# Kernel optimization log

Hardware: AMD Instinct MI355X
Metric: run time of the kernel (lower is better)

The kernel has to match this reference:

```python
import jax, jax.numpy as jnp
import numpy as np

MU_P = 0.15
MASK_ID = 103
VOCAB = 30522


def setup_inputs() -> dict:
    key = jax.random.key(0)
    k1, k2 = jax.random.split(key)
    B, C, S = 1024, 4, 2048
    # first half = per-token sampling weights, second half = shared_tokens (unused by the math)
    my_attention_mask = jax.random.uniform(k1, (B, C, 2 * S), dtype=jnp.float32)
    attention_mask = jnp.ones((B, C, S), dtype=jnp.int32)  # tokenizer attention mask
    input_ids = jax.random.randint(k2, (B, C, S), 0, VOCAB, dtype=jnp.int32)
    return {"my_attention_mask": my_attention_mask,
            "attention_mask": attention_mask,
            "input_ids": input_ids}


def reference(my_attention_mask, attention_mask, input_ids):
    """Weighted sampling WITHOUT replacement per (batch, choice) row via Gumbel-top-k.

    Original loops over (k, j), draws num_to_mask = floor(sum(tok_mask) * N(mu_p, sigma))
    indices from the nonzero weights in my_attention_mask[..., :S] (prob ~ weight),
    masks those token positions in input_ids and emits the indicator mask.
    Gumbel-top-k: keys = log(w) + Gumbel noise; the top-num_to_mask keys are a
    weighted sample without replacement from w. Zero-weight positions get -inf keys.
    """
    B, C, S = input_ids.shape
    w = my_attention_mask[..., :S]  # [B, C, S] sampling weights

    key = jax.random.key(42)
    kg, kn = jax.random.split(key)
    sigma = min(0.05, MU_P / 4.0)
    frac = MU_P + sigma * jax.random.normal(kn, (B, C), dtype=jnp.float32)
    num_to_mask = jnp.floor(
        attention_mask.sum(axis=-1).astype(jnp.float32) * frac
    ).astype(jnp.int32)  # [B, C]

    log_w = jnp.where(w > 0, jnp.log(jnp.maximum(w, 1e-30)), -jnp.inf)
    keys = log_w + jax.random.gumbel(kg, w.shape, dtype=jnp.float32)  # [B, C, S]

    # rank[i] = position of i in descending key order (double argsort)
    order = jnp.argsort(-keys, axis=-1)
    rank = jnp.argsort(order, axis=-1)
    new_attention_mask = (rank < num_to_mask[..., None]).astype(jnp.int32)  # [B, C, S]

    new_input_ids = jnp.where(new_attention_mask == 1, MASK_ID, input_ids)
    discriminator_labels = -new_attention_mask
    return new_input_ids, new_attention_mask, discriminator_labels
```

## Files before the change

kernel.cpp:

```cpp
#include <hip/hip_runtime.h>
#include <stdint.h>
#include <math.h>

#define SLEN 2048
#define EPT 8
#define NTHREADS 256
#define TOKENS_PER_OUT 8388608

__host__ __device__ __forceinline__ void tf2x32(uint32_t k0, uint32_t k1,
                                                uint32_t x0, uint32_t x1,
                                                uint32_t &o0, uint32_t &o1) {
  uint32_t ks2 = 0x1BD11BDAu ^ k0 ^ k1;
  x0 += k0; x1 += k1;
#define TFR(r) { x0 += x1; x1 = (x1 << (r)) | (x1 >> (32 - (r))); x1 ^= x0; }
  TFR(13) TFR(15) TFR(26) TFR(6)
  x0 += k1;  x1 += ks2 + 1u;
  TFR(17) TFR(29) TFR(16) TFR(24)
  x0 += ks2; x1 += k0 + 2u;
  TFR(13) TFR(15) TFR(26) TFR(6)
  x0 += k0;  x1 += k1 + 3u;
  TFR(17) TFR(29) TFR(16) TFR(24)
  x0 += k1;  x1 += ks2 + 4u;
  TFR(13) TFR(15) TFR(26) TFR(6)
  x0 += ks2; x1 += k0 + 5u;
#undef TFR
  o0 = x0; o1 = x1;
}

__device__ __forceinline__ float u01_from_bits(uint32_t bits) {
  return __uint_as_float((bits >> 9) | 0x3F800000u) - 1.0f;
}

__device__ __forceinline__ float log_cr(float x) {
  double d = (double)x;
  long long b = __double_as_longlong(d);
  int e = (int)(b >> 52) - 1023;
  double m = __longlong_as_double((b & 0x000FFFFFFFFFFFFFLL) | 0x3FF0000000000000LL);
  if (m > 1.4142135623730951) { m *= 0.5; e += 1; }
  double r = (m - 1.0) / (m + 1.0);
  double t = r * r;
  double p = 0.07692307692307693;
  p = fma(p, t, 0.09090909090909091);
  p = fma(p, t, 0.1111111111111111);
  p = fma(p, t, 0.14285714285714285);
  p = fma(p, t, 0.2);
  p = fma(p, t, 0.3333333333333333);
  double q = fma(p, t, 1.0);
  return (float)fma((double)e, 0.6931471805599453, 2.0 * (r * q));
}

__device__ float erfinv_xla(float x) {
#pragma clang fp contract(off)
  float x2  = x * x;
  float nx2 = -x2;
  float l1p;
  if (fabsf(nx2) < 1e-4f) {
    l1p = (-0.5f * nx2 + 1.0f) * nx2;
  } else {
    l1p = log_cr(1.0f + nx2);
  }
  float w = -l1p;
  float p;
  if (w < 5.0f) {
    float ww = w - 2.5f;
    p = 2.81022636e-08f;
    p = p * ww + 3.43273939e-07f;
    p = p * ww + -3.5233877e-06f;
    p = p * ww + -4.39150654e-06f;
    p = p * ww + 0.00021858087f;
    p = p * ww + -0.00125372503f;
    p = p * ww + -0.00417768164f;
    p = p * ww + 0.246640727f;
    p = p * ww + 1.50140941f;
  } else {
    float ww = sqrtf(w) - 3.0f;
    p = -0.000200214257f;
    p = p * ww + 0.000100950558f;
    p = p * ww + 0.00134934322f;
    p = p * ww + -0.00367342844f;
    p = p * ww + 0.00573950773f;
    p = p * ww + -0.0076224613f;
    p = p * ww + 0.00943887047f;
    p = p * ww + 1.00167406f;
    p = p * ww + 2.83297682f;
  }
  return p * x;
}

__global__ __launch_bounds__(NTHREADS)
void gumbel_topk_mask(const float* __restrict__ wfull,
                      const int*   __restrict__ attn,
                      const int*   __restrict__ ids,
                      int* __restrict__ out,
                      uint32_t kg0, uint32_t kg1, uint32_t kn0, uint32_t kn1) {
#pragma clang fp contract(off)
  const int row  = blockIdx.x;
  const int t    = threadIdx.x;
  const int lane = t & 63;
  const int wid  = t >> 6;

  __shared__ __align__(16) uint32_t hist[256];
  __shared__ uint32_t wsum[4];
  __shared__ int      kk_s;
  __shared__ uint32_t prefix_s;
  __shared__ uint32_t remaining_s;

  const size_t rbase = (size_t)row * SLEN;
  const size_t wbase = (size_t)row * (2 * SLEN);
  const int    base  = t * EPT;

  const float4* wv4 = (const float4*)(wfull + wbase + base);
  float4 w0 = wv4[0], w1 = wv4[1];
  const int4* av4 = (const int4*)(attn + rbase + base);
  int4 a0 = av4[0], a1 = av4[1];
  int psum = a0.x + a0.y + a0.z + a0.w + a1.x + a1.y + a1.z + a1.w;

  float wl[EPT] = {w0.x, w0.y, w0.z, w0.w, w1.x, w1.y, w1.z, w1.w};
  uint32_t mloc[EPT];
#pragma unroll
  for (int e = 0; e < EPT; ++e) {
    uint32_t o0, o1;
    tf2x32(kg0, kg1, 0u, (uint32_t)(rbase + base + e), o0, o1);
    float f  = u01_from_bits(o0 ^ o1);
    float uu = fmaxf(1.17549435e-38f, f * 1.0f + 1.17549435e-38f);
    float g  = -log_cr(-log_cr(uu));
    float w  = wl[e];
    float key = (w > 0.0f) ? (log_cr(fmaxf(w, 1e-30f)) + g) : -__builtin_inff();
    uint32_t kb = __float_as_uint(key);
    mloc[e] = (kb & 0x80000000u) ? ~kb : (kb | 0x80000000u);
  }

#pragma unroll
  for (int off = 32; off; off >>= 1) psum += __shfl_down(psum, off, 64);
  if (lane == 0) wsum[wid] = (uint32_t)psum;
  __syncthreads();

  if (t == 0) {
    int asum = (int)(wsum[0] + wsum[1] + wsum[2] + wsum[3]);
    uint32_t o0, o1;
    tf2x32(kn0, kn1, 0u, (uint32_t)row, o0, o1);
    float f   = u01_from_bits(o0 ^ o1);
    float lo  = __uint_as_float(0xBF7FFFFFu);
    float u2  = fmaxf(lo, f * 2.0f + lo);
    float z   = erfinv_xla(u2);
    float nrm = 1.4142135623730951f * z;
    float frac = 0.15f + 0.0375f * nrm;
    float fnum = (float)asum * frac;
    int kk = (int)floorf(fnum);
    kk_s = kk;
    prefix_s = 0u;
    remaining_s = (uint32_t)(kk < 0 ? 0 : kk);
  }
  __syncthreads();

  int kk = kk_s;
  uint32_t T, r;
  if (kk <= 0)         { T = 0xFFFFFFFFu; r = 0u; }
  else if (kk >= SLEN) { T = 0u;          r = SLEN; }
  else {
    for (int p = 3; p >= 0; --p) {
      hist[t] = 0u;
      __syncthreads();
      uint32_t pref = prefix_s;
      if (p == 3) {
#pragma unroll
        for (int e = 0; e < EPT; ++e) atomicAdd(&hist[mloc[e] >> 24], 1u);
      } else {
        uint32_t sh = (uint32_t)(8 * (p + 1));
#pragma unroll
        for (int e = 0; e < EPT; ++e) {
          uint32_t m = mloc[e];
          if ((m >> sh) == (pref >> sh)) atomicAdd(&hist[(m >> (8 * p)) & 255u], 1u);
        }
      }
      __syncthreads();
      if (t < 64) {
        uint32_t need = remaining_s;
        uint4 hq = ((const uint4*)hist)[t];
        uint32_t gs  = hq.x + hq.y + hq.z + hq.w;
        uint32_t sfx = gs;
#pragma unroll
        for (int off = 1; off < 64; off <<= 1) {
          uint32_t n = __shfl_down(sfx, off, 64);
          if (t + off < 64) sfx += n;
        }
        uint32_t Gex = sfx - gs;
        uint32_t S3 = Gex;
        uint32_t S2 = S3 + hq.w;
        uint32_t S1 = S2 + hq.z;
        uint32_t S0 = S1 + hq.y;
        uint32_t hh[4] = {hq.x, hq.y, hq.z, hq.w};
        uint32_t SS[4] = {S0, S1, S2, S3};
#pragma unroll
        for (int i = 0; i < 4; ++i) {
          if (hh[i] && SS[i] < need && need <= SS[i] + hh[i]) {
            prefix_s |= ((uint32_t)(4 * t + i)) << (8 * p);
            remaining_s = need - SS[i];
          }
        }
      }
      __syncthreads();
    }
    T = prefix_s;
    r = remaining_s;
  }

  int local_eq = 0;
#pragma unroll
  for (int e = 0; e < EPT; ++e) local_eq += (mloc[e] == T) ? 1 : 0;
  uint32_t v = (uint32_t)local_eq;
#pragma unroll
  for (int off = 1; off < 64; off <<= 1) {
    uint32_t n = __shfl_up(v, off, 64);
    if (lane >= off) v += n;
  }
  if (lane == 63) wsum[wid] = v;
  __syncthreads();
  uint32_t add = 0;
  for (int i = 0; i < wid; ++i) add += wsum[i];
  uint32_t excl = add + v - (uint32_t)local_eq;

  const int4* iv4 = (const int4*)(ids + rbase + base);
  int4 i0 = iv4[0], i1 = iv4[1];
  int idv[EPT] = {i0.x, i0.y, i0.z, i0.w, i1.x, i1.y, i1.z, i1.w};
  int oid[EPT], omk[EPT], olb[EPT];
#pragma unroll
  for (int e = 0; e < EPT; ++e) {
    uint32_t m = mloc[e];
    bool eq  = (m == T);
    bool msk = (m > T) || (eq && (excl < r));
    excl += eq ? 1u : 0u;
    oid[e] = msk ? 103 : idv[e];
    omk[e] = msk ? 1 : 0;
    olb[e] = msk ? -1 : 0;
  }
  int4* po = (int4*)(out + rbase + base);
  po[0] = make_int4(oid[0], oid[1], oid[2], oid[3]);
  po[1] = make_int4(oid[4], oid[5], oid[6], oid[7]);
  int4* pm = (int4*)(out + TOKENS_PER_OUT + rbase + base);
  pm[0] = make_int4(omk[0], omk[1], omk[2], omk[3]);
  pm[1] = make_int4(omk[4], omk[5], omk[6], omk[7]);
  int4* pl = (int4*)(out + 2 * TOKENS_PER_OUT + rbase + base);
  pl[0] = make_int4(olb[0], olb[1], olb[2], olb[3]);
  pl[1] = make_int4(olb[4], olb[5], olb[6], olb[7]);
}

extern "C" void kernel_launch(void* const* d_in, const int* in_sizes, int n_in,
                              void* d_out, int out_size, void* d_ws, size_t ws_size,
                              hipStream_t stream) {
  (void)n_in; (void)d_ws; (void)ws_size; (void)out_size;
  const float* wfull = (const float*)d_in[0];
  const int*   attn  = (const int*)d_in[1];
  const int*   ids   = (const int*)d_in[2];
  int* out = (int*)d_out;

  uint32_t kg0, kg1, kn0, kn1, o0, o1;
  tf2x32(0u, 42u, 0u, 0u, o0, o1); kg0 = o0; kg1 = o1;
  tf2x32(0u, 42u, 0u, 1u, o0, o1); kn0 = o0; kn1 = o1;

  int rows = in_sizes[1] / SLEN;
  hipLaunchKernelGGL(gumbel_topk_mask, dim3(rows), dim3(NTHREADS), 0, stream,
                     wfull, attn, ids, out, kg0, kg1, kn0, kn1);
}
```

Before: 204.0 us.

## Double-buffer radix histograms, early-exit select, and cheapen log division

```diff
diff --git a/kernel.cpp b/kernel.cpp
--- a/kernel.cpp
+++ b/kernel.cpp
@@ -32,12 +32,17 @@
 }
 
 __device__ __forceinline__ float log_cr(float x) {
+#pragma clang fp contract(off)
   double d = (double)x;
   long long b = __double_as_longlong(d);
   int e = (int)(b >> 52) - 1023;
   double m = __longlong_as_double((b & 0x000FFFFFFFFFFFFFLL) | 0x3FF0000000000000LL);
   if (m > 1.4142135623730951) { m *= 0.5; e += 1; }
-  double r = (m - 1.0) / (m + 1.0);
+  double mp1 = m + 1.0;
+  double y = __builtin_amdgcn_rcp(mp1);
+  y = fma(fma(-mp1, y, 1.0), y, y);
+  y = fma(fma(-mp1, y, 1.0), y, y);
+  double r = (m - 1.0) * y;
   double t = r * r;
   double p = 0.07692307692307693;
   p = fma(p, t, 0.09090909090909091);
@@ -87,7 +92,7 @@
   return p * x;
 }
 
-__global__ __launch_bounds__(NTHREADS)
+__global__ __launch_bounds__(NTHREADS, 6)
 void gumbel_topk_mask(const float* __restrict__ wfull,
                       const int*   __restrict__ attn,
                       const int*   __restrict__ ids,
@@ -99,29 +104,40 @@
   const int lane = t & 63;
   const int wid  = t >> 6;
 
-  __shared__ __align__(16) uint32_t hist[256];
+  __shared__ __align__(16) uint32_t hist[2][256];
   __shared__ uint32_t wsum[4];
-  __shared__ int      kk_s;
   __shared__ uint32_t prefix_s;
   __shared__ uint32_t remaining_s;
+  __shared__ int      done_s;
 
   const size_t rbase = (size_t)row * SLEN;
   const size_t wbase = (size_t)row * (2 * SLEN);
   const int    base  = t * EPT;
+
+  hist[0][t] = 0u;
+  hist[1][t] = 0u;
 
   const float4* wv4 = (const float4*)(wfull + wbase + base);
   float4 w0 = wv4[0], w1 = wv4[1];
   const int4* av4 = (const int4*)(attn + rbase + base);
   int4 a0 = av4[0], a1 = av4[1];
+  const int4* iv4 = (const int4*)(ids + rbase + base);
+  int4 i0 = iv4[0], i1 = iv4[1];
   int psum = a0.x + a0.y + a0.z + a0.w + a1.x + a1.y + a1.z + a1.w;
 
-  float wl[EPT] = {w0.x, w0.y, w0.z, w0.w, w1.x, w1.y, w1.z, w1.w};
-  uint32_t mloc[EPT];
+  uint32_t bits[EPT];
 #pragma unroll
   for (int e = 0; e < EPT; ++e) {
     uint32_t o0, o1;
     tf2x32(kg0, kg1, 0u, (uint32_t)(rbase + base + e), o0, o1);
-    float f  = u01_from_bits(o0 ^ o1);
+    bits[e] = o0 ^ o1;
+  }
+
+  float wl[EPT] = {w0.x, w0.y, w0.z, w0.w, w1.x, w1.y, w1.z, w1.w};
+  uint32_t mloc[EPT];
+#pragma unroll
+  for (int e = 0; e < EPT; ++e) {
+    float f  = u01_from_bits(bits[e]);
     float uu = fmaxf(1.17549435e-38f, f * 1.0f + 1.17549435e-38f);
     float g  = -log_cr(-log_cr(uu));
     float w  = wl[e];
@@ -133,50 +149,36 @@
 #pragma unroll
   for (int off = 32; off; off >>= 1) psum += __shfl_down(psum, off, 64);
   if (lane == 0) wsum[wid] = (uint32_t)psum;
+  if (t == 0) { prefix_s = 0u; done_s = 0; }
   __syncthreads();
 
-  if (t == 0) {
-    int asum = (int)(wsum[0] + wsum[1] + wsum[2] + wsum[3]);
-    uint32_t o0, o1;
-    tf2x32(kn0, kn1, 0u, (uint32_t)row, o0, o1);
-    float f   = u01_from_bits(o0 ^ o1);
-    float lo  = __uint_as_float(0xBF7FFFFFu);
-    float u2  = fmaxf(lo, f * 2.0f + lo);
-    float z   = erfinv_xla(u2);
-    float nrm = 1.4142135623730951f * z;
-    float frac = 0.15f + 0.0375f * nrm;
-    float fnum = (float)asum * frac;
-    int kk = (int)floorf(fnum);
-    kk_s = kk;
-    prefix_s = 0u;
-    remaining_s = (uint32_t)(kk < 0 ? 0 : kk);
-  }
-  __syncthreads();
-
-  int kk = kk_s;
-  uint32_t T, r;
-  if (kk <= 0)         { T = 0xFFFFFFFFu; r = 0u; }
-  else if (kk >= SLEN) { T = 0u;          r = SLEN; }
-  else {
-    for (int p = 3; p >= 0; --p) {
-      hist[t] = 0u;
-      __syncthreads();
-      uint32_t pref = prefix_s;
+#pragma unroll
+  for (int e = 0; e < EPT; ++e) atomicAdd(&hist[0][mloc[e] >> 24], 1u);
+
+  int cur = 0;
+  for (int p = 3; p >= 0; --p) {
+    __syncthreads();
+    if (t < 64) {
+      uint32_t need = 0u;
       if (p == 3) {
-#pragma unroll
-        for (int e = 0; e < EPT; ++e) atomicAdd(&hist[mloc[e] >> 24], 1u);
+        int asum = (int)(wsum[0] + wsum[1] + wsum[2] + wsum[3]);
+        uint32_t o0, o1;
+        tf2x32(kn0, kn1, 0u, (uint32_t)row, o0, o1);
+        float f   = u01_from_bits(o0 ^ o1);
+        float lo  = __uint_as_float(0xBF7FFFFFu);
+        float u2  = fmaxf(lo, f * 2.0f + lo);
+        float z   = erfinv_xla(u2);
+        float nrm = 1.4142135623730951f * z;
+        float frac = 0.15f + 0.0375f * nrm;
+        int kk = (int)floorf((float)asum * frac);
+        if (kk <= 0)         { if (t == 0) { prefix_s = 0xFFFFFFFFu; remaining_s = 0u;   done_s = 1; } }
+        else if (kk >= SLEN) { if (t == 0) { prefix_s = 0u;          remaining_s = SLEN; done_s = 1; } }
+        else need = (uint32_t)kk;
       } else {
-        uint32_t sh = (uint32_t)(8 * (p + 1));
-#pragma unroll
-        for (int e = 0; e < EPT; ++e) {
-          uint32_t m = mloc[e];
-          if ((m >> sh) == (pref >> sh)) atomicAdd(&hist[(m >> (8 * p)) & 255u], 1u);
-        }
+        need = remaining_s;
       }
-      __syncthreads();
-      if (t < 64) {
-        uint32_t need = remaining_s;
-        uint4 hq = ((const uint4*)hist)[t];
+      if (need) {
+        uint4 hq = ((const uint4*)hist[cur])[t];
         uint32_t gs  = hq.x + hq.y + hq.z + hq.w;
         uint32_t sfx = gs;
 #pragma unroll
@@ -195,15 +197,33 @@
         for (int i = 0; i < 4; ++i) {
           if (hh[i] && SS[i] < need && need <= SS[i] + hh[i]) {
             prefix_s |= ((uint32_t)(4 * t + i)) << (8 * p);
-            remaining_s = need - SS[i];
+            uint32_t rem = need - SS[i];
+            remaining_s = rem;
+            if (rem == hh[i]) done_s = 1;
           }
         }
       }
-      __syncthreads();
+    } else {
+      int idx = t - 64;
+      hist[cur ^ 1][idx] = 0u;
+      if (idx < 64) hist[cur ^ 1][idx + 192] = 0u;
     }
-    T = prefix_s;
-    r = remaining_s;
-  }
+    __syncthreads();
+    if (done_s) break;
+    if (p > 0) {
+      uint32_t pref = prefix_s;
+      int sh = 8 * p;
+#pragma unroll
+      for (int e = 0; e < EPT; ++e) {
+        uint32_t m = mloc[e];
+        if ((m >> sh) == (pref >> sh))
+          atomicAdd(&hist[cur ^ 1][(m >> (sh - 8)) & 255u], 1u);
+      }
+    }
+    cur ^= 1;
+  }
+  uint32_t T = prefix_s;
+  uint32_t r = remaining_s;
 
   int local_eq = 0;
 #pragma unroll
@@ -220,8 +240,6 @@
   for (int i = 0; i < wid; ++i) add += wsum[i];
   uint32_t excl = add + v - (uint32_t)local_eq;
 
-  const int4* iv4 = (const int4*)(ids + rbase + base);
-  int4 i0 = iv4[0], i1 = iv4[1];
   int idv[EPT] = {i0.x, i0.y, i0.z, i0.w, i1.x, i1.y, i1.z, i1.w};
   int oid[EPT], omk[EPT], olb[EPT];
 #pragma unroll
```

New measurement: 206.7 us. About the same (+1.3%).

## Process each row with a single wavefront to eliminate block barriers

Applied to the files above, without the earlier changes.

```diff
diff --git a/kernel.cpp b/kernel.cpp
--- a/kernel.cpp
+++ b/kernel.cpp
@@ -3,8 +3,6 @@
 #include <math.h>
 
 #define SLEN 2048
-#define EPT 8
-#define NTHREADS 256
 #define TOKENS_PER_OUT 8388608
 
 __host__ __device__ __forceinline__ void tf2x32(uint32_t k0, uint32_t k1,
@@ -32,12 +30,16 @@
 }
 
 __device__ __forceinline__ float log_cr(float x) {
+#pragma clang fp contract(off)
   double d = (double)x;
   long long b = __double_as_longlong(d);
   int e = (int)(b >> 52) - 1023;
   double m = __longlong_as_double((b & 0x000FFFFFFFFFFFFFLL) | 0x3FF0000000000000LL);
   if (m > 1.4142135623730951) { m *= 0.5; e += 1; }
-  double r = (m - 1.0) / (m + 1.0);
+  double mp1 = m + 1.0;
+  double y = __builtin_amdgcn_rcp(mp1);
+  y = fma(fma(-mp1, y, 1.0), y, y);
+  double r = (m - 1.0) * y;
   double t = r * r;
   double p = 0.07692307692307693;
   p = fma(p, t, 0.09090909090909091);
@@ -87,7 +89,7 @@
   return p * x;
 }
 
-__global__ __launch_bounds__(NTHREADS)
+__global__ __launch_bounds__(64, 4)
 void gumbel_topk_mask(const float* __restrict__ wfull,
                       const int*   __restrict__ attn,
                       const int*   __restrict__ ids,
@@ -95,48 +97,45 @@
                       uint32_t kg0, uint32_t kg1, uint32_t kn0, uint32_t kn1) {
 #pragma clang fp contract(off)
   const int row  = blockIdx.x;
-  const int t    = threadIdx.x;
-  const int lane = t & 63;
-  const int wid  = t >> 6;
-
+  const int lane = threadIdx.x;
+
+  __shared__ __align__(16) uint32_t mk[SLEN];
   __shared__ __align__(16) uint32_t hist[256];
-  __shared__ uint32_t wsum[4];
-  __shared__ int      kk_s;
-  __shared__ uint32_t prefix_s;
-  __shared__ uint32_t remaining_s;
 
   const size_t rbase = (size_t)row * SLEN;
   const size_t wbase = (size_t)row * (2 * SLEN);
-  const int    base  = t * EPT;
-
-  const float4* wv4 = (const float4*)(wfull + wbase + base);
-  float4 w0 = wv4[0], w1 = wv4[1];
-  const int4* av4 = (const int4*)(attn + rbase + base);
-  int4 a0 = av4[0], a1 = av4[1];
-  int psum = a0.x + a0.y + a0.z + a0.w + a1.x + a1.y + a1.z + a1.w;
-
-  float wl[EPT] = {w0.x, w0.y, w0.z, w0.w, w1.x, w1.y, w1.z, w1.w};
-  uint32_t mloc[EPT];
-#pragma unroll
-  for (int e = 0; e < EPT; ++e) {
-    uint32_t o0, o1;
-    tf2x32(kg0, kg1, 0u, (uint32_t)(rbase + base + e), o0, o1);
-    float f  = u01_from_bits(o0 ^ o1);
-    float uu = fmaxf(1.17549435e-38f, f * 1.0f + 1.17549435e-38f);
-    float g  = -log_cr(-log_cr(uu));
-    float w  = wl[e];
-    float key = (w > 0.0f) ? (log_cr(fmaxf(w, 1e-30f)) + g) : -__builtin_inff();
-    uint32_t kb = __float_as_uint(key);
-    mloc[e] = (kb & 0x80000000u) ? ~kb : (kb | 0x80000000u);
-  }
-
-#pragma unroll
-  for (int off = 32; off; off >>= 1) psum += __shfl_down(psum, off, 64);
-  if (lane == 0) wsum[wid] = (uint32_t)psum;
-  __syncthreads();
-
-  if (t == 0) {
-    int asum = (int)(wsum[0] + wsum[1] + wsum[2] + wsum[3]);
+
+  ((uint4*)hist)[lane] = make_uint4(0u, 0u, 0u, 0u);
+
+  int psum = 0;
+  for (int e = 0; e < 8; ++e) {
+    const int c = e * 64 + lane;
+    float4 wv = ((const float4*)(wfull + wbase))[c];
+    int4   av = ((const int4*)(attn + rbase))[c];
+    psum += av.x + av.y + av.z + av.w;
+    float wl[4] = {wv.x, wv.y, wv.z, wv.w};
+    uint32_t mv[4];
+#pragma unroll
+    for (int j = 0; j < 4; ++j) {
+      uint32_t o0, o1;
+      tf2x32(kg0, kg1, 0u, (uint32_t)(rbase + 4 * c + j), o0, o1);
+      float f  = u01_from_bits(o0 ^ o1);
+      float uu = fmaxf(1.17549435e-38f, f * 1.0f + 1.17549435e-38f);
+      float g  = -log_cr(-log_cr(uu));
+      float key = (wl[j] > 0.0f) ? (log_cr(fmaxf(wl[j], 1e-30f)) + g)
+                                 : -__builtin_inff();
+      uint32_t kb = __float_as_uint(key);
+      mv[j] = (kb & 0x80000000u) ? ~kb : (kb | 0x80000000u);
+      atomicAdd(&hist[mv[j] >> 24], 1u);
+    }
+    ((uint4*)mk)[c] = make_uint4(mv[0], mv[1], mv[2], mv[3]);
+  }
+
+#pragma unroll
+  for (int off = 32; off; off >>= 1) psum += __shfl_xor(psum, off, 64);
+
+  int kk;
+  {
     uint32_t o0, o1;
     tf2x32(kn0, kn1, 0u, (uint32_t)row, o0, o1);
     float f   = u01_from_bits(o0 ^ o1);
@@ -145,104 +144,90 @@
     float z   = erfinv_xla(u2);
     float nrm = 1.4142135623730951f * z;
     float frac = 0.15f + 0.0375f * nrm;
-    float fnum = (float)asum * frac;
-    int kk = (int)floorf(fnum);
-    kk_s = kk;
-    prefix_s = 0u;
-    remaining_s = (uint32_t)(kk < 0 ? 0 : kk);
-  }
-  __syncthreads();
-
-  int kk = kk_s;
+    kk = (int)floorf((float)psum * frac);
+  }
+
   uint32_t T, r;
   if (kk <= 0)         { T = 0xFFFFFFFFu; r = 0u; }
   else if (kk >= SLEN) { T = 0u;          r = SLEN; }
   else {
-    for (int p = 3; p >= 0; --p) {
-      hist[t] = 0u;
-      __syncthreads();
-      uint32_t pref = prefix_s;
-      if (p == 3) {
-#pragma unroll
-        for (int e = 0; e < EPT; ++e) atomicAdd(&hist[mloc[e] >> 24], 1u);
-      } else {
-        uint32_t sh = (uint32_t)(8 * (p + 1));
-#pragma unroll
-        for (int e = 0; e < EPT; ++e) {
-          uint32_t m = mloc[e];
-          if ((m >> sh) == (pref >> sh)) atomicAdd(&hist[(m >> (8 * p)) & 255u], 1u);
+    uint32_t need = (uint32_t)kk, prefix = 0u;
+    for (int p = 3;; --p) {
+      uint4 hq = ((const uint4*)hist)[lane];
+      uint32_t hh[4] = {hq.x, hq.y, hq.z, hq.w};
+      uint32_t gs  = hh[0] + hh[1] + hh[2] + hh[3];
+      uint32_t sfx = gs;
+#pragma unroll
+      for (int off = 1; off < 64; off <<= 1) {
+        uint32_t n = __shfl_down(sfx, off, 64);
+        if (lane + off < 64) sfx += n;
+      }
+      uint32_t Gex = sfx - gs;
+      uint32_t SS[4];
+      SS[3] = Gex;
+      SS[2] = SS[3] + hh[3];
+      SS[1] = SS[2] + hh[2];
+      SS[0] = SS[1] + hh[1];
+      int win = -1; uint32_t wrem = 0u, wcnt = 0u;
+#pragma unroll
+      for (int i = 0; i < 4; ++i) {
+        if (hh[i] && SS[i] < need && need <= SS[i] + hh[i]) {
+          win = 4 * lane + i; wrem = need - SS[i]; wcnt = hh[i];
         }
       }
-      __syncthreads();
-      if (t < 64) {
-        uint32_t need = remaining_s;
-        uint4 hq = ((const uint4*)hist)[t];
-        uint32_t gs  = hq.x + hq.y + hq.z + hq.w;
-        uint32_t sfx = gs;
-#pragma unroll
-        for (int off = 1; off < 64; off <<= 1) {
-          uint32_t n = __shfl_down(sfx, off, 64);
-          if (t + off < 64) sfx += n;
-        }
-        uint32_t Gex = sfx - gs;
-        uint32_t S3 = Gex;
-        uint32_t S2 = S3 + hq.w;
-        uint32_t S1 = S2 + hq.z;
-        uint32_t S0 = S1 + hq.y;
-        uint32_t hh[4] = {hq.x, hq.y, hq.z, hq.w};
-        uint32_t SS[4] = {S0, S1, S2, S3};
-#pragma unroll
-        for (int i = 0; i < 4; ++i) {
-          if (hh[i] && SS[i] < need && need <= SS[i] + hh[i]) {
-            prefix_s |= ((uint32_t)(4 * t + i)) << (8 * p);
-            remaining_s = need - SS[i];
-          }
-        }
+      unsigned long long bal = __ballot(win >= 0);
+      int wl_ = __ffsll(bal) - 1;
+      prefix |= ((uint32_t)__shfl(win, wl_, 64)) << (8 * p);
+      need = (uint32_t)__shfl((int)wrem, wl_, 64);
+      uint32_t cnt = (uint32_t)__shfl((int)wcnt, wl_, 64);
+      if (p == 0 || need == cnt) break;
+      ((uint4*)hist)[lane] = make_uint4(0u, 0u, 0u, 0u);
+      const int sh = 8 * p;
+      for (int e = 0; e < 8; ++e) {
+        uint4 mq = ((const uint4*)mk)[e * 64 + lane];
+        uint32_t mm[4] = {mq.x, mq.y, mq.z, mq.w};
+#pragma unroll
+        for (int j = 0; j < 4; ++j)
+          if ((mm[j] >> sh) == (prefix >> sh))
+            atomicAdd(&hist[(mm[j] >> (sh - 8)) & 255u], 1u);
       }
-      __syncthreads();
-    }
-    T = prefix_s;
-    r = remaining_s;
-  }
-
-  int local_eq = 0;
-#pragma unroll
-  for (int e = 0; e < EPT; ++e) local_eq += (mloc[e] == T) ? 1 : 0;
-  uint32_t v = (uint32_t)local_eq;
-#pragma unroll
-  for (int off = 1; off < 64; off <<= 1) {
-    uint32_t n = __shfl_up(v, off, 64);
-    if (lane >= off) v += n;
-  }
-  if (lane == 63) wsum[wid] = v;
-  __syncthreads();
-  uint32_t add = 0;
-  for (int i = 0; i < wid; ++i) add += wsum[i];
-  uint32_t excl = add + v - (uint32_t)local_eq;
-
-  const int4* iv4 = (const int4*)(ids + rbase + base);
-  int4 i0 = iv4[0], i1 = iv4[1];
-  int idv[EPT] = {i0.x, i0.y, i0.z, i0.w, i1.x, i1.y, i1.z, i1.w};
-  int oid[EPT], omk[EPT], olb[EPT];
-#pragma unroll
-  for (int e = 0; e < EPT; ++e) {
-    uint32_t m = mloc[e];
-    bool eq  = (m == T);
-    bool msk = (m > T) || (eq && (excl < r));
-    excl += eq ? 1u : 0u;
-    oid[e] = msk ? 103 : idv[e];
-    omk[e] = msk ? 1 : 0;
-    olb[e] = msk ? -1 : 0;
-  }
-  int4* po = (int4*)(out + rbase + base);
-  po[0] = make_int4(oid[0], oid[1], oid[2], oid[3]);
-  po[1] = make_int4(oid[4], oid[5], oid[6], oid[7]);
-  int4* pm = (int4*)(out + TOKENS_PER_OUT + rbase + base);
-  pm[0] = make_int4(omk[0], omk[1], omk[2], omk[3]);
-  pm[1] = make_int4(omk[4], omk[5], omk[6], omk[7]);
-  int4* pl = (int4*)(out + 2 * TOKENS_PER_OUT + rbase + base);
-  pl[0] = make_int4(olb[0], olb[1], olb[2], olb[3]);
-  pl[1] = make_int4(olb[4], olb[5], olb[6], olb[7]);
+    }
+    T = prefix;
+    r = need;
+  }
+
+  const unsigned long long lt = (1ull << lane) - 1ull;
+  uint32_t total = 0u;
+  for (int e = 0; e < 8; ++e) {
+    const int c = e * 64 + lane;
+    uint4 mq = ((const uint4*)mk)[c];
+    int4  iv = ((const int4*)(ids + rbase))[c];
+    uint32_t mm[4] = {mq.x, mq.y, mq.z, mq.w};
+    bool eq[4];
+    uint32_t cross = 0u, slot_tot = 0u;
+#pragma unroll
+    for (int j = 0; j < 4; ++j) {
+      eq[j] = (mm[j] == T);
+      unsigned long long bj = __ballot(eq[j]);
+      cross    += (uint32_t)__popcll(bj & lt);
+      slot_tot += (uint32_t)__popcll(bj);
+    }
+    uint32_t excl = total + cross;
+    total += slot_tot;
+    int o_[4], m_[4], l_[4];
+    int idv[4] = {iv.x, iv.y, iv.z, iv.w};
+#pragma unroll
+    for (int j = 0; j < 4; ++j) {
+      bool msk = (mm[j] > T) || (eq[j] && (excl < r));
+      excl += eq[j] ? 1u : 0u;
+      o_[j] = msk ? 103 : idv[j];
+      m_[j] = msk ? 1 : 0;
+      l_[j] = msk ? -1 : 0;
+    }
+    ((int4*)(out + rbase))[c]                    = make_int4(o_[0], o_[1], o_[2], o_[3]);
+    ((int4*)(out + TOKENS_PER_OUT + rbase))[c]   = make_int4(m_[0], m_[1], m_[2], m_[3]);
+    ((int4*)(out + 2 * TOKENS_PER_OUT + rbase))[c] = make_int4(l_[0], l_[1], l_[2], l_[3]);
+  }
 }
 
 extern "C" void kernel_launch(void* const* d_in, const int* in_sizes, int n_in,
@@ -259,6 +244,6 @@
   tf2x32(0u, 42u, 0u, 1u, o0, o1); kn0 = o0; kn1 = o1;
 
   int rows = in_sizes[1] / SLEN;
-  hipLaunchKernelGGL(gumbel_topk_mask, dim3(rows), dim3(NTHREADS), 0, stream,
+  hipLaunchKernelGGL(gumbel_topk_mask, dim3(rows), dim3(64), 0, stream,
                      wfull, attn, ids, out, kg0, kg1, kn0, kn1);
 }
```

Result: slower. 212.7 us (+4.3%).
